# Kernel tuning notes

Hardware: AMD Instinct MI355X
Metric: run time of the kernel (lower is better)

The kernel has to match this reference:

```python
import jax, jax.numpy as jnp
import numpy as np

BETA = 0.25
N_CODEBOOK = 2  # hard-coded in the original module
EPS = 1e-12     # torch F.normalize default eps


def l2norm(t):
    # matches torch.nn.functional.normalize(t, p=2, dim=-1)
    n = jnp.linalg.norm(t, axis=-1, keepdims=True)
    return t / jnp.maximum(n, EPS)


def setup_inputs() -> dict:
    key = jax.random.key(0)
    k1, k2 = jax.random.split(key)
    b, n, e_dim, n_e = 16, 256, 1024, 4096
    c = e_dim // N_CODEBOOK
    z = jax.random.normal(k1, (b, n, e_dim), dtype=jnp.float32)
    emb_weight = jax.random.normal(k2, (N_CODEBOOK * n_e, c), dtype=jnp.float32)
    return {"z": z, "emb_weight": emb_weight}


def reference(z, emb_weight):
    b, n, e_dim = z.shape
    f = N_CODEBOOK
    c = e_dim // f
    n_e = emb_weight.shape[0] // f

    # 'b n (f c) -> b f n c'
    zf = jnp.transpose(z.reshape(b, n, f, c), (0, 2, 1, 3))
    # '(b f) c -> b f c' with b=2 (codebooks), f=n_e
    protos = emb_weight.reshape(f, n_e, c)

    zn = l2norm(zf)            # (b, f, n, c)
    pn = l2norm(protos)        # (f, m, c)

    # cosine distance; batch repeat of prototypes is a pure broadcast
    d = 2.0 - 2.0 * jnp.einsum('bfnc,fmc->bfnm', zn, pn)  # (b, f, n, m)
    encoding_indices = jnp.argmin(d, axis=-1)              # (b, f, n) in [0, n_e)

    # faithful to source: indices gather from the FULL (2*n_e) table, no offset
    z_q = l2norm(emb_weight[encoding_indices])             # (b, f, n, c)

    sg = jax.lax.stop_gradient
    loss = BETA * jnp.mean((sg(z_q) - zn) ** 2) + jnp.mean((z_q - sg(zn)) ** 2)

    z_q_st = zn + sg(z_q - zn)                             # straight-through
    # 'b f n c -> b n (f c)'
    z_q_out = jnp.transpose(z_q_st, (0, 2, 1, 3)).reshape(b, n, e_dim)
    return z_q_out, loss, encoding_indices
```

## Files before the change

### kernel.cpp

```cpp
#include <hip/hip_runtime.h>
#include <hip/hip_bf16.h>
#include <stdint.h>

#define FCB 2
#define BB 16
#define NN 256
#define EDIM 1024
#define CC 512
#define NE 4096
#define TOKENS (BB*FCB*NN)
#define ROWS (FCB*NE)
#define OUT_LOSS (BB*NN*EDIM)
#define OUT_IDX  (OUT_LOSS + 1)
#define MARGIN 0.15f

typedef __attribute__((ext_vector_type(8))) short bf16x8;
typedef __attribute__((ext_vector_type(4))) float f32x4;

__device__ __forceinline__ unsigned int ford(float v) {
    unsigned int u = __float_as_uint(v);
    return (u & 0x80000000u) ? ~u : (u | 0x80000000u);
}
__device__ __forceinline__ float unford(unsigned int u) {
    unsigned int b = (u & 0x80000000u) ? (u & 0x7fffffffu) : ~u;
    return __uint_as_float(b);
}


__global__ __launch_bounds__(256) void pack_hi(
    const float* __restrict__ z, const float* __restrict__ emb,
    short* __restrict__ z_hi, short* __restrict__ e_hi,
    float* __restrict__ norm_sq)
{
    __shared__ float red[256];
    int bid = blockIdx.x;
    int tid = threadIdx.x;
    bool is_emb = (bid >= 2048);
    const float* src; short* hi; int RS, FRO, FCO;
    if (!is_emb) { src = z;   hi = z_hi; RS = EDIM; FRO = 0;  FCO = CC; }
    else         { src = emb; hi = e_hi; RS = CC;   FRO = NE; FCO = 0; bid -= 2048; }
    int u = bid * 256 + tid;
    int m = u & 15;
    int Q = (u >> 4) & 63;
    int R = (u >> 10) & 255;
    int f = u >> 18;
    int row = R * 16 + m;
    const float* s = src + (size_t)(f * FRO + row) * RS + f * FCO + Q * 8;
    float4 v0 = *(const float4*)s;
    float4 v1 = *(const float4*)(s + 4);
    float vv[8] = {v0.x, v0.y, v0.z, v0.w, v1.x, v1.y, v1.z, v1.w};
    bf16x8 h8;
    float ss = 0.f;
    #pragma unroll
    for (int j = 0; j < 8; ++j) {
        __hip_bfloat16 hb = __float2bfloat16(vv[j]);
        h8[j] = *(short*)&hb;
        ss = fmaf(vv[j], vv[j], ss);
    }
    *(bf16x8*)(hi + (size_t)u * 8) = h8;

    if (is_emb) {
        red[tid] = ss;
        __syncthreads();
        if (tid < 16) {
            float t = 0.f;
            #pragma unroll
            for (int q = 0; q < 16; ++q) t += red[tid + 16 * q];
            int bf = (bid * 256) >> 18;
            int bR = ((bid * 256) >> 10) & 255;
            atomicAdd(norm_sq + bf * NE + bR * 16 + tid, t);
        }
    }
}

__global__ __launch_bounds__(256, 3) void gemm_sel(
    const short* __restrict__ zh, const short* __restrict__ eh,
    const float* __restrict__ norm_sq, unsigned int* __restrict__ cand)
{
    __shared__ char smem[32768];
    const int f  = blockIdx.z;
    const int t0 = blockIdx.y * 128;
    const int m0 = blockIdx.x * 128;
    const int tid  = threadIdx.x;
    const int wave = tid >> 6, lane = tid & 63;
    const int wm = wave & 1, wn = wave >> 1;

    f32x4 acc[4][4] = {};

    for (int step = 0; step < 8; ++step) {
        __syncthreads();
        #pragma unroll
        for (int i = 0; i < 8; ++i) {
            int c = wave * 8 + i;
            const short* gsrc = (c < 16) ? zh : eh;
            int cl = c & 15;
            int Rl = cl >> 1, h = cl & 1;
            int R = ((c < 16) ? (t0 >> 4) : (m0 >> 4)) + Rl;
            int qb = step * 8 + h * 4;
            const short* g = gsrc
                + (((size_t)f * 256 + R) * 64 + qb) * 128 + (size_t)lane * 8;
            __builtin_amdgcn_global_load_lds(
                (const __attribute__((address_space(1))) void*)g,
                (__attribute__((address_space(3))) void*)(smem + c * 1024),
                16, 0, 0);
        }
        __syncthreads();

        #pragma unroll
        for (int h = 0; h < 2; ++h) {
            bf16x8 ah[4], bh[4];
            #pragma unroll
            for (int i = 0; i < 4; ++i) {
                ah[i] = *(const bf16x8*)(smem + ((wm*4 + i)*2 + h) * 1024 + lane * 16);
                bh[i] = *(const bf16x8*)(smem + 16384 + ((wn*4 + i)*2 + h) * 1024 + lane * 16);
            }
            #pragma unroll
            for (int i = 0; i < 4; ++i)
                #pragma unroll
                for (int j2 = 0; j2 < 4; ++j2)
                    acc[i][j2] = __builtin_amdgcn_mfma_f32_16x16x32_bf16(ah[i], bh[j2], acc[i][j2], 0, 0, 0);
        }
    }

    float inm[4]; unsigned ccode[4];
    #pragma unroll
    for (int j2 = 0; j2 < 4; ++j2) {
        int col = j2 * 16 + (lane & 15);
        ccode[j2] = (unsigned)(col ^ 63);
        inm[j2] = rsqrtf(norm_sq[f * NE + m0 + wn * 64 + col]);
    }

    #pragma unroll
    for (int i = 0; i < 4; ++i) {
        #pragma unroll
        for (int r = 0; r < 4; ++r) {
            unsigned p1 = 0u, p2 = 0u;
            #pragma unroll
            for (int j2 = 0; j2 < 4; ++j2) {
                float w = acc[i][j2][r] * inm[j2];
                unsigned pw = (ford(w) & 0xFFFFFFC0u) | ccode[j2];
                if (pw > p1) { p2 = p1; p1 = pw; }
                else if (pw > p2) p2 = pw;
            }
            #pragma unroll
            for (int off = 8; off; off >>= 1) {
                unsigned q1 = __shfl_down(p1, off, 16);
                unsigned q2 = __shfl_down(p2, off, 16);
                if (q1 > p1) { unsigned t = p1; p1 = q1; p2 = (t > q2) ? t : q2; }
                else         { p2 = (p2 > q1) ? p2 : q1; }
            }
            if ((lane & 15) == 0) {
                int u = t0 + wm * 64 + i * 16 + (lane >> 4) * 4 + r;
                int b = u >> 8, n = u & 255;
                int gt = ((b * FCB + f) << 8) + n;
                int s = (blockIdx.x << 1) | wn;
                uint2 val; val.x = p1; val.y = p2;
                *(uint2*)(cand + ((size_t)gt << 7) + (s << 1)) = val;
            }
        }
    }
}

__global__ __launch_bounds__(256) void rescore_epilogue(
    const float* __restrict__ z, const float* __restrict__ emb,
    const unsigned int* __restrict__ cand,
    float* __restrict__ out, float* __restrict__ loss_tok)
{
    int t = blockIdx.x * 4 + (threadIdx.x >> 6);
    int lane = threadIdx.x & 63;
    int n = t & 255;
    int f = (t >> 8) & 1;
    int b = t >> 9;
    const float* zrow = z + ((size_t)(b*NN + n))*EDIM + f*CC;
    float4 za = *(const float4*)(zrow + lane * 8);
    float4 zb = *(const float4*)(zrow + lane * 8 + 4);

    uint2 cc = *(const uint2*)(cand + ((size_t)t << 7) + (lane << 1));
    unsigned c1 = cc.x, c2 = cc.y;

    unsigned m1 = (c1 > c2) ? c1 : c2;
    #pragma unroll
    for (int off = 32; off; off >>= 1) {
        unsigned o = __shfl_xor(m1, off);
        if (o > m1) m1 = o;
    }
    float thr = unford(m1) - MARGIN;

    unsigned long long bestp = 0ull;
    #pragma unroll
    for (int rnd = 0; rnd < 2; ++rnd) {
        unsigned u = rnd ? c2 : c1;
        float v = unford(u);
        unsigned long long mask = __ballot(v > thr);
        while (mask) {
            int src = __ffsll((long long)mask) - 1;
            mask &= mask - 1;
            unsigned cu = __shfl(u, src);
            int idx = (src << 6) | ((int)(cu & 63u) ^ 63);
            const float* er = emb + ((size_t)(f * NE + idx)) * CC;
            float4 ea = *(const float4*)(er + lane * 8);
            float4 eb = *(const float4*)(er + lane * 8 + 4);
            float d  = za.x*ea.x + za.y*ea.y + za.z*ea.z + za.w*ea.w
                     + zb.x*eb.x + zb.y*eb.y + zb.z*eb.z + zb.w*eb.w;
            float se = ea.x*ea.x + ea.y*ea.y + ea.z*ea.z + ea.w*ea.w
                     + eb.x*eb.x + eb.y*eb.y + eb.z*eb.z + eb.w*eb.w;
            #pragma unroll
            for (int off = 32; off; off >>= 1) {
                d  += __shfl_xor(d, off);
                se += __shfl_xor(se, off);
            }
            float vex = d / fmaxf(sqrtf(se), 1e-12f);
            unsigned long long pex = ((unsigned long long)ford(vex) << 32)
                                   | (unsigned int)(~(unsigned int)idx);
            if (pex > bestp) bestp = pex;
        }
    }
    int idxb = (int)(~(unsigned int)bestp);

    const float* er0 = emb + (size_t)idxb * CC;
    float4 ea = *(const float4*)(er0 + lane * 8);
    float4 eb = *(const float4*)(er0 + lane * 8 + 4);
    float se0 = ea.x*ea.x + ea.y*ea.y + ea.z*ea.z + ea.w*ea.w
              + eb.x*eb.x + eb.y*eb.y + eb.z*eb.z + eb.w*eb.w;
    #pragma unroll
    for (int off = 32; off; off >>= 1) se0 += __shfl_xor(se0, off);
    float inm0 = 1.0f / fmaxf(sqrtf(se0), 1e-12f);
    float* orow = out + ((size_t)(b*NN + n))*EDIM + f*CC;
    ea.x *= inm0; ea.y *= inm0; ea.z *= inm0; ea.w *= inm0;
    eb.x *= inm0; eb.y *= inm0; eb.z *= inm0; eb.w *= inm0;
    *(float4*)(orow + lane * 8) = ea;
    *(float4*)(orow + lane * 8 + 4) = eb;
    float s1 = za.x*za.x + za.y*za.y + za.z*za.z + za.w*za.w
             + zb.x*zb.x + zb.y*zb.y + zb.z*zb.z + zb.w*zb.w;
    float s2 = za.x*ea.x + za.y*ea.y + za.z*ea.z + za.w*ea.w
             + zb.x*eb.x + zb.y*eb.y + zb.z*eb.z + zb.w*eb.w;
    #pragma unroll
    for (int off = 32; off; off >>= 1) {
        s1 += __shfl_xor(s1, off);
        s2 += __shfl_xor(s2, off);
    }
    if (lane == 0) {
        float cosv = s2 / fmaxf(sqrtf(s1), 1e-12f);
        loss_tok[t] = 2.0f - 2.0f * cosv;
        out[OUT_IDX + t] = (float)idxb;
    }
}

__global__ __launch_bounds__(256) void loss_reduce(
    const float* __restrict__ loss_tok, float* __restrict__ out)
{
    int tid = threadIdx.x;
    float s = 0.f;
    #pragma unroll
    for (int h = 0; h < 32; ++h) s += loss_tok[h * 256 + tid];
    #pragma unroll
    for (int off = 32; off; off >>= 1) s += __shfl_down(s, off);
    __shared__ float part[4];
    if ((tid & 63) == 0) part[tid >> 6] = s;
    __syncthreads();
    if (tid == 0) {
        float t = part[0] + part[1] + part[2] + part[3];
        out[OUT_LOSS] = t * (1.25f / (float)OUT_LOSS);
    }
}

extern "C" void kernel_launch(void* const* d_in, const int* in_sizes, int n_in,
                              void* d_out, int out_size, void* d_ws, size_t ws_size,
                              hipStream_t stream) {
    const float* z   = (const float*)d_in[0];
    const float* emb = (const float*)d_in[1];
    float* out = (float*)d_out;

    char* ws = (char*)d_ws;
    float* norm_sq = (float*)ws;
    unsigned int* cand = (unsigned int*)(ws + 32768);
    float* loss_tok = (float*)(ws + 32768 + (size_t)4*1024*1024);
    short* z_hi = (short*)(ws + 65536 + (size_t)4*1024*1024);
    short* e_hi = z_hi + (size_t)FCB * NE * CC;

    hipMemsetAsync(norm_sq, 0, ROWS * sizeof(float), stream);
    pack_hi<<<4096, 256, 0, stream>>>(z, emb, z_hi, e_hi, norm_sq);
    gemm_sel<<<dim3(NE/128, NE/128, FCB), 256, 0, stream>>>(z_hi, e_hi, norm_sq, cand);
    rescore_epilogue<<<TOKENS/4, 256, 0, stream>>>(z, emb, cand, out, loss_tok);
    loss_reduce<<<1, 256, 0, stream>>>(loss_tok, out);
}
```

Baseline: 146.3 us.

## Enlarge similarity GEMM tile to 256x256 with double-buffered async LDS pipeline

Rewrites the bf16 similarity GEMM to use 256x256 block tiles with 8 waves. The main loop is now software-pipelined: global_load_lds prefetches the next K-chunk into a second 64KB LDS buffer while MFMAs run on the current one. Fine-grained vmcnt waits, explicit barriers and s_setprio bracket the MFMA bursts. The aim is to raise operand reuse and hide global-load latency. In exchange it uses 128KB of LDS per block, which limits occupancy to one block per CU, and halves the grid size, so tail effects can grow.

```diff
diff --git a/kernel.cpp b/kernel.cpp
--- a/kernel.cpp
+++ b/kernel.cpp
@@ -25,6 +25,11 @@
     unsigned int b = (u & 0x80000000u) ? (u & 0x7fffffffu) : ~u;
     return __uint_as_float(b);
 }
+
+__device__ __forceinline__ void vm8()   { asm volatile("s_waitcnt vmcnt(8)" ::: "memory"); }
+__device__ __forceinline__ void vm4()   { asm volatile("s_waitcnt vmcnt(4)" ::: "memory"); }
+__device__ __forceinline__ void vm0()   { asm volatile("s_waitcnt vmcnt(0)" ::: "memory"); }
+__device__ __forceinline__ void lgkm0() { asm volatile("s_waitcnt lgkmcnt(0)" ::: "memory"); }
 
 
 __global__ __launch_bounds__(256) void pack_hi(
@@ -73,72 +78,137 @@
     }
 }
 
-__global__ __launch_bounds__(256, 3) void gemm_sel(
+__global__ __launch_bounds__(512, 2) void gemm_sel(
     const short* __restrict__ zh, const short* __restrict__ eh,
     const float* __restrict__ norm_sq, unsigned int* __restrict__ cand)
 {
-    __shared__ char smem[32768];
+    __shared__ __attribute__((aligned(128))) char smem[131072];
     const int f  = blockIdx.z;
-    const int t0 = blockIdx.y * 128;
-    const int m0 = blockIdx.x * 128;
+    const int t0 = blockIdx.y * 256;
+    const int m0 = blockIdx.x * 256;
     const int tid  = threadIdx.x;
     const int wave = tid >> 6, lane = tid & 63;
     const int wm = wave & 1, wn = wave >> 1;
 
-    f32x4 acc[4][4] = {};
-
-    for (int step = 0; step < 8; ++step) {
-        __syncthreads();
-        #pragma unroll
-        for (int i = 0; i < 8; ++i) {
-            int c = wave * 8 + i;
-            const short* gsrc = (c < 16) ? zh : eh;
-            int cl = c & 15;
-            int Rl = cl >> 1, h = cl & 1;
-            int R = ((c < 16) ? (t0 >> 4) : (m0 >> 4)) + Rl;
-            int qb = step * 8 + h * 4;
-            const short* g = gsrc
-                + (((size_t)f * 256 + R) * 64 + qb) * 128 + (size_t)lane * 8;
+    const int cbA = (f * 256 + (t0 >> 4)) * 64;
+    const int cbB = (f * 256 + (m0 >> 4)) * 64;
+
+    f32x4 acc[8][4] = {};
+
+    auto stage_half = [&](const short* __restrict__ gsrc, int chunk0, char* dst) {
+        #pragma unroll
+        for (int i = 0; i < 2; ++i) {
+            int Rp = wave * 2 + i;
+            const short* g = gsrc + ((size_t)(chunk0 + Rp * 64)) * 128 + (size_t)lane * 8;
             __builtin_amdgcn_global_load_lds(
                 (const __attribute__((address_space(1))) void*)g,
-                (__attribute__((address_space(3))) void*)(smem + c * 1024),
-                16, 0, 0);
+                (__attribute__((address_space(3))) void*)(dst + Rp * 1024), 16, 0, 0);
         }
-        __syncthreads();
-
-        #pragma unroll
-        for (int h = 0; h < 2; ++h) {
-            bf16x8 ah[4], bh[4];
-            #pragma unroll
-            for (int i = 0; i < 4; ++i) {
-                ah[i] = *(const bf16x8*)(smem + ((wm*4 + i)*2 + h) * 1024 + lane * 16);
-                bh[i] = *(const bf16x8*)(smem + 16384 + ((wn*4 + i)*2 + h) * 1024 + lane * 16);
-            }
-            #pragma unroll
-            for (int i = 0; i < 4; ++i)
-                #pragma unroll
-                for (int j2 = 0; j2 < 4; ++j2)
-                    acc[i][j2] = __builtin_amdgcn_mfma_f32_16x16x32_bf16(ah[i], bh[j2], acc[i][j2], 0, 0, 0);
-        }
+    };
+
+    stage_half(zh, cbA + 0,     smem + 0);
+    stage_half(eh, cbB + 0,     smem + 32768);
+    stage_half(zh, cbA + 4,     smem + 16384);
+    stage_half(eh, cbB + 4,     smem + 32768 + 16384);
+    stage_half(zh, cbA + 8,     smem + 65536);
+    stage_half(eh, cbB + 8,     smem + 65536 + 32768);
+    vm8();
+    __builtin_amdgcn_s_barrier();
+
+    #pragma unroll
+    for (int t = 0; t < 8; ++t) {
+        char* cur = smem + (t & 1) * 65536;
+        char* nxt = smem + ((t + 1) & 1) * 65536;
+        const char* curA = cur;
+        const char* curB = cur + 32768;
+        bf16x8 af[4], bf[4];
+
+        #pragma unroll
+        for (int nj = 0; nj < 4; ++nj)
+            bf[nj] = *(const bf16x8*)(curB + (wn * 4 + nj) * 1024 + lane * 16);
+        #pragma unroll
+        for (int mi = 0; mi < 4; ++mi)
+            af[mi] = *(const bf16x8*)(curA + (wm * 8 + mi) * 1024 + lane * 16);
+        if (t < 7) stage_half(zh, cbA + (t + 1) * 8 + 4, nxt + 16384);
+        __builtin_amdgcn_s_barrier();
+        lgkm0();
+        __builtin_amdgcn_s_setprio(1);
+        #pragma unroll
+        for (int mi = 0; mi < 4; ++mi)
+            #pragma unroll
+            for (int nj = 0; nj < 4; ++nj)
+                acc[mi][nj] = __builtin_amdgcn_mfma_f32_16x16x32_bf16(af[mi], bf[nj], acc[mi][nj], 0, 0, 0);
+        __builtin_amdgcn_s_setprio(0);
+        __builtin_amdgcn_s_barrier();
+
+        #pragma unroll
+        for (int mi = 0; mi < 4; ++mi)
+            af[mi] = *(const bf16x8*)(curA + (wm * 8 + 4 + mi) * 1024 + lane * 16);
+        if (t < 7) stage_half(eh, cbB + (t + 1) * 8 + 4, nxt + 32768 + 16384);
+        if (t < 7) vm8(); else vm0();
+        __builtin_amdgcn_s_barrier();
+        lgkm0();
+        __builtin_amdgcn_s_setprio(1);
+        #pragma unroll
+        for (int mi = 0; mi < 4; ++mi)
+            #pragma unroll
+            for (int nj = 0; nj < 4; ++nj)
+                acc[4 + mi][nj] = __builtin_amdgcn_mfma_f32_16x16x32_bf16(af[mi], bf[nj], acc[4 + mi][nj], 0, 0, 0);
+        __builtin_amdgcn_s_setprio(0);
+        __builtin_amdgcn_s_barrier();
+
+        #pragma unroll
+        for (int nj = 0; nj < 4; ++nj)
+            bf[nj] = *(const bf16x8*)(curB + 16384 + (wn * 4 + nj) * 1024 + lane * 16);
+        #pragma unroll
+        for (int mi = 0; mi < 4; ++mi)
+            af[mi] = *(const bf16x8*)(curA + 16384 + (wm * 8 + mi) * 1024 + lane * 16);
+        if (t < 6) stage_half(zh, cbA + (t + 2) * 8, cur);
+        __builtin_amdgcn_s_barrier();
+        lgkm0();
+        __builtin_amdgcn_s_setprio(1);
+        #pragma unroll
+        for (int mi = 0; mi < 4; ++mi)
+            #pragma unroll
+            for (int nj = 0; nj < 4; ++nj)
+                acc[mi][nj] = __builtin_amdgcn_mfma_f32_16x16x32_bf16(af[mi], bf[nj], acc[mi][nj], 0, 0, 0);
+        __builtin_amdgcn_s_setprio(0);
+        __builtin_amdgcn_s_barrier();
+
+        #pragma unroll
+        for (int mi = 0; mi < 4; ++mi)
+            af[mi] = *(const bf16x8*)(curA + 16384 + (wm * 8 + 4 + mi) * 1024 + lane * 16);
+        if (t < 6) stage_half(eh, cbB + (t + 2) * 8, cur + 32768);
+        if (t < 6) vm8(); else if (t == 6) vm4();
+        __builtin_amdgcn_s_barrier();
+        lgkm0();
+        __builtin_amdgcn_s_setprio(1);
+        #pragma unroll
+        for (int mi = 0; mi < 4; ++mi)
+            #pragma unroll
+            for (int nj = 0; nj < 4; ++nj)
+                acc[4 + mi][nj] = __builtin_amdgcn_mfma_f32_16x16x32_bf16(af[mi], bf[nj], acc[4 + mi][nj], 0, 0, 0);
+        __builtin_amdgcn_s_setprio(0);
+        __builtin_amdgcn_s_barrier();
     }
 
     float inm[4]; unsigned ccode[4];
     #pragma unroll
-    for (int j2 = 0; j2 < 4; ++j2) {
-        int col = j2 * 16 + (lane & 15);
-        ccode[j2] = (unsigned)(col ^ 63);
-        inm[j2] = rsqrtf(norm_sq[f * NE + m0 + wn * 64 + col]);
-    }
-
-    #pragma unroll
-    for (int i = 0; i < 4; ++i) {
+    for (int nj = 0; nj < 4; ++nj) {
+        int col = nj * 16 + (lane & 15);
+        ccode[nj] = (unsigned)(col ^ 63);
+        inm[nj] = rsqrtf(norm_sq[f * NE + m0 + wn * 64 + col]);
+    }
+
+    #pragma unroll
+    for (int mi = 0; mi < 8; ++mi) {
         #pragma unroll
         for (int r = 0; r < 4; ++r) {
             unsigned p1 = 0u, p2 = 0u;
             #pragma unroll
-            for (int j2 = 0; j2 < 4; ++j2) {
-                float w = acc[i][j2][r] * inm[j2];
-                unsigned pw = (ford(w) & 0xFFFFFFC0u) | ccode[j2];
+            for (int nj = 0; nj < 4; ++nj) {
+                float w = acc[mi][nj][r] * inm[nj];
+                unsigned pw = (ford(w) & 0xFFFFFFC0u) | ccode[nj];
                 if (pw > p1) { p2 = p1; p1 = pw; }
                 else if (pw > p2) p2 = pw;
             }
@@ -146,14 +216,14 @@
             for (int off = 8; off; off >>= 1) {
                 unsigned q1 = __shfl_down(p1, off, 16);
                 unsigned q2 = __shfl_down(p2, off, 16);
-                if (q1 > p1) { unsigned t = p1; p1 = q1; p2 = (t > q2) ? t : q2; }
+                if (q1 > p1) { unsigned tt = p1; p1 = q1; p2 = (tt > q2) ? tt : q2; }
                 else         { p2 = (p2 > q1) ? p2 : q1; }
             }
             if ((lane & 15) == 0) {
-                int u = t0 + wm * 64 + i * 16 + (lane >> 4) * 4 + r;
+                int u = t0 + wm * 128 + mi * 16 + (lane >> 4) * 4 + r;
                 int b = u >> 8, n = u & 255;
                 int gt = ((b * FCB + f) << 8) + n;
-                int s = (blockIdx.x << 1) | wn;
+                int s = (blockIdx.x << 2) | wn;
                 uint2 val; val.x = p1; val.y = p2;
                 *(uint2*)(cand + ((size_t)gt << 7) + (s << 1)) = val;
             }
@@ -280,7 +350,7 @@
 
     hipMemsetAsync(norm_sq, 0, ROWS * sizeof(float), stream);
     pack_hi<<<4096, 256, 0, stream>>>(z, emb, z_hi, e_hi, norm_sq);
-    gemm_sel<<<dim3(NE/128, NE/128, FCB), 256, 0, stream>>>(z_hi, e_hi, norm_sq, cand);
+    gemm_sel<<<dim3(NE/256, NE/256, FCB), 512, 0, stream>>>(z_hi, e_hi, norm_sq, cand);
     rescore_epilogue<<<TOKENS/4, 256, 0, stream>>>(z, emb, cand, out, loss_tok);
     loss_reduce<<<1, 256, 0, stream>>>(loss_tok, out);
 }
```

New measurement: 144.3 us. About the same (-1.3%).

## Double-buffer GEMM LDS staging with 256-token tiles and fuse loss reduction via atomics

Applied to the files above, without the earlier changes.

The selection GEMM now uses 512-thread blocks covering 256 tokens by 128 codebook rows. LDS staging is split into two half-buffers so the next K-step's global-to-LDS loads are issued before the current MFMAs run, which is meant to hide load latency and drop one barrier per step. The separate loss-reduce kernel is removed: each token atomically adds its scaled loss into the output after a memset, saving a launch. The cost is more LDS per block and heavier register pressure, plus a nondeterministic float atomic sum contended by all 8192 tokens.

```diff
diff --git a/kernel.cpp b/kernel.cpp
--- a/kernel.cpp
+++ b/kernel.cpp
@@ -73,72 +73,81 @@
     }
 }
 
-__global__ __launch_bounds__(256, 3) void gemm_sel(
+__global__ __launch_bounds__(512, 4) void gemm_sel(
     const short* __restrict__ zh, const short* __restrict__ eh,
     const float* __restrict__ norm_sq, unsigned int* __restrict__ cand)
 {
-    __shared__ char smem[32768];
+    __shared__ __attribute__((aligned(128))) char smem[49152];
     const int f  = blockIdx.z;
-    const int t0 = blockIdx.y * 128;
+    const int t0 = blockIdx.y * 256;
     const int m0 = blockIdx.x * 128;
     const int tid  = threadIdx.x;
     const int wave = tid >> 6, lane = tid & 63;
-    const int wm = wave & 1, wn = wave >> 1;
+    const int wm = wave & 3, wn = wave >> 2;
 
     f32x4 acc[4][4] = {};
 
-    for (int step = 0; step < 8; ++step) {
-        __syncthreads();
+    auto stage = [&](int t, int h) {
+        int qb = t * 8 + h * 4;
+        char* base = smem + h * 24576;
         #pragma unroll
-        for (int i = 0; i < 8; ++i) {
-            int c = wave * 8 + i;
-            const short* gsrc = (c < 16) ? zh : eh;
-            int cl = c & 15;
-            int Rl = cl >> 1, h = cl & 1;
-            int R = ((c < 16) ? (t0 >> 4) : (m0 >> 4)) + Rl;
-            int qb = step * 8 + h * 4;
-            const short* g = gsrc
-                + (((size_t)f * 256 + R) * 64 + qb) * 128 + (size_t)lane * 8;
+        for (int i = 0; i < 2; ++i) {
+            int Rl = wave * 2 + i;
+            const short* g = zh + (((size_t)f * 256 + (t0 >> 4) + Rl) * 64 + qb) * 128
+                           + (size_t)lane * 8;
             __builtin_amdgcn_global_load_lds(
                 (const __attribute__((address_space(1))) void*)g,
-                (__attribute__((address_space(3))) void*)(smem + c * 1024),
-                16, 0, 0);
-        }
-        __syncthreads();
-
+                (__attribute__((address_space(3))) void*)(base + Rl * 1024), 16, 0, 0);
+        }
+        const short* g = eh + (((size_t)f * 256 + (m0 >> 4) + wave) * 64 + qb) * 128
+                       + (size_t)lane * 8;
+        __builtin_amdgcn_global_load_lds(
+            (const __attribute__((address_space(1))) void*)g,
+            (__attribute__((address_space(3))) void*)(base + 16384 + wave * 1024), 16, 0, 0);
+    };
+
+    stage(0, 0);
+    stage(0, 1);
+    __syncthreads();
+
+    for (int t = 0; t < 8; ++t) {
         #pragma unroll
         for (int h = 0; h < 2; ++h) {
-            bf16x8 ah[4], bh[4];
-            #pragma unroll
-            for (int i = 0; i < 4; ++i) {
-                ah[i] = *(const bf16x8*)(smem + ((wm*4 + i)*2 + h) * 1024 + lane * 16);
-                bh[i] = *(const bf16x8*)(smem + 16384 + ((wn*4 + i)*2 + h) * 1024 + lane * 16);
-            }
-            #pragma unroll
-            for (int i = 0; i < 4; ++i)
+            const char* base = smem + h * 24576;
+            bf16x8 af[4], bfr[4];
+            #pragma unroll
+            for (int mi = 0; mi < 4; ++mi)
+                af[mi] = *(const bf16x8*)(base + (wm * 4 + mi) * 1024 + lane * 16);
+            #pragma unroll
+            for (int nj = 0; nj < 4; ++nj)
+                bfr[nj] = *(const bf16x8*)(base + 16384 + (wn * 4 + nj) * 1024 + lane * 16);
+            __syncthreads();
+            if (t < 7) stage(t + 1, h);
+            #pragma unroll
+            for (int mi = 0; mi < 4; ++mi)
                 #pragma unroll
-                for (int j2 = 0; j2 < 4; ++j2)
-                    acc[i][j2] = __builtin_amdgcn_mfma_f32_16x16x32_bf16(ah[i], bh[j2], acc[i][j2], 0, 0, 0);
+                for (int nj = 0; nj < 4; ++nj)
+                    acc[mi][nj] = __builtin_amdgcn_mfma_f32_16x16x32_bf16(af[mi], bfr[nj], acc[mi][nj], 0, 0, 0);
         }
     }
 
     float inm[4]; unsigned ccode[4];
     #pragma unroll
-    for (int j2 = 0; j2 < 4; ++j2) {
-        int col = j2 * 16 + (lane & 15);
-        ccode[j2] = (unsigned)(col ^ 63);
-        inm[j2] = rsqrtf(norm_sq[f * NE + m0 + wn * 64 + col]);
-    }
-
-    #pragma unroll
-    for (int i = 0; i < 4; ++i) {
+    for (int nj = 0; nj < 4; ++nj) {
+        int col = nj * 16 + (lane & 15);
+        ccode[nj] = (unsigned)(col ^ 63);
+        inm[nj] = rsqrtf(norm_sq[f * NE + m0 + wn * 64 + col]);
+    }
+
+    #pragma unroll
+    for (int mi = 0; mi < 4; ++mi) {
         #pragma unroll
         for (int r = 0; r < 4; ++r) {
             unsigned p1 = 0u, p2 = 0u;
             #pragma unroll
-            for (int j2 = 0; j2 < 4; ++j2) {
-                float w = acc[i][j2][r] * inm[j2];
-                unsigned pw = (ford(w) & 0xFFFFFFC0u) | ccode[j2];
+            for (int nj = 0; nj < 4; ++nj) {
+                float w = acc[mi][nj][r] * inm[nj];
+                unsigned pw = (ford(w) & 0xFFFFFFC0u) | ccode[nj];
                 if (pw > p1) { p2 = p1; p1 = pw; }
                 else if (pw > p2) p2 = pw;
             }
@@ -146,11 +155,11 @@
             for (int off = 8; off; off >>= 1) {
                 unsigned q1 = __shfl_down(p1, off, 16);
                 unsigned q2 = __shfl_down(p2, off, 16);
-                if (q1 > p1) { unsigned t = p1; p1 = q1; p2 = (t > q2) ? t : q2; }
+                if (q1 > p1) { unsigned tt = p1; p1 = q1; p2 = (tt > q2) ? tt : q2; }
                 else         { p2 = (p2 > q1) ? p2 : q1; }
             }
             if ((lane & 15) == 0) {
-                int u = t0 + wm * 64 + i * 16 + (lane >> 4) * 4 + r;
+                int u = t0 + wm * 64 + mi * 16 + (lane >> 4) * 4 + r;
                 int b = u >> 8, n = u & 255;
                 int gt = ((b * FCB + f) << 8) + n;
                 int s = (blockIdx.x << 1) | wn;
@@ -163,8 +172,7 @@
 
 __global__ __launch_bounds__(256) void rescore_epilogue(
     const float* __restrict__ z, const float* __restrict__ emb,
-    const unsigned int* __restrict__ cand,
-    float* __restrict__ out, float* __restrict__ loss_tok)
+    const unsigned int* __restrict__ cand, float* __restrict__ out)
 {
     int t = blockIdx.x * 4 + (threadIdx.x >> 6);
     int lane = threadIdx.x & 63;
@@ -241,26 +249,9 @@
     }
     if (lane == 0) {
         float cosv = s2 / fmaxf(sqrtf(s1), 1e-12f);
-        loss_tok[t] = 2.0f - 2.0f * cosv;
+        float loss = 2.0f - 2.0f * cosv;
+        atomicAdd(out + OUT_LOSS, loss * (1.25f / (float)OUT_LOSS));
         out[OUT_IDX + t] = (float)idxb;
-    }
-}
-
-__global__ __launch_bounds__(256) void loss_reduce(
-    const float* __restrict__ loss_tok, float* __restrict__ out)
-{
-    int tid = threadIdx.x;
-    float s = 0.f;
-    #pragma unroll
-    for (int h = 0; h < 32; ++h) s += loss_tok[h * 256 + tid];
-    #pragma unroll
-    for (int off = 32; off; off >>= 1) s += __shfl_down(s, off);
-    __shared__ float part[4];
-    if ((tid & 63) == 0) part[tid >> 6] = s;
-    __syncthreads();
-    if (tid == 0) {
-        float t = part[0] + part[1] + part[2] + part[3];
-        out[OUT_LOSS] = t * (1.25f / (float)OUT_LOSS);
     }
 }
 
@@ -274,13 +265,12 @@
     char* ws = (char*)d_ws;
     float* norm_sq = (float*)ws;
     unsigned int* cand = (unsigned int*)(ws + 32768);
-    float* loss_tok = (float*)(ws + 32768 + (size_t)4*1024*1024);
     short* z_hi = (short*)(ws + 65536 + (size_t)4*1024*1024);
     short* e_hi = z_hi + (size_t)FCB * NE * CC;
 
     hipMemsetAsync(norm_sq, 0, ROWS * sizeof(float), stream);
+    hipMemsetAsync(out + OUT_LOSS, 0, sizeof(float), stream);
     pack_hi<<<4096, 256, 0, stream>>>(z, emb, z_hi, e_hi, norm_sq);
-    gemm_sel<<<dim3(NE/128, NE/128, FCB), 256, 0, stream>>>(z_hi, e_hi, norm_sq, cand);
-    rescore_epilogue<<<TOKENS/4, 256, 0, stream>>>(z, emb, cand, out, loss_tok);
-    loss_reduce<<<1, 256, 0, stream>>>(loss_tok, out);
-}
+    gemm_sel<<<dim3(NE/128, 4096/256, FCB), 512, 0, stream>>>(z_hi, e_hi, norm_sq, cand);
+    rescore_epilogue<<<TOKENS/4, 256, 0, stream>>>(z, emb, cand, out);
+}
```

New measurement: 242.3 us. +65.6%, slower.

## Double-buffer GEMM LDS staging and reuse precomputed norms in rescore

Applied to the files above, without the earlier changes.

Splits the GEMM's shared-memory tile into two buffers so the next K-step's global-to-LDS loads are issued before computing on the current buffer. Launch bounds are relaxed from 3 to 2 blocks per CU to fit the doubled LDS. The rescore kernel now reads squared codebook norms already accumulated by the pack kernel, instead of recomputing and reducing them for each candidate and for the final row. The tradeoff is lower occupancy in the GEMM, and the norms come from an atomic accumulation rather than a direct reduction.

```diff
diff --git a/kernel.cpp b/kernel.cpp
--- a/kernel.cpp
+++ b/kernel.cpp
@@ -73,11 +73,11 @@
     }
 }
 
-__global__ __launch_bounds__(256, 3) void gemm_sel(
+__global__ __launch_bounds__(256, 2) void gemm_sel(
     const short* __restrict__ zh, const short* __restrict__ eh,
     const float* __restrict__ norm_sq, unsigned int* __restrict__ cand)
 {
-    __shared__ char smem[32768];
+    __shared__ __attribute__((aligned(128))) char smem[2][32768];
     const int f  = blockIdx.z;
     const int t0 = blockIdx.y * 128;
     const int m0 = blockIdx.x * 128;
@@ -87,8 +87,7 @@
 
     f32x4 acc[4][4] = {};
 
-    for (int step = 0; step < 8; ++step) {
-        __syncthreads();
+    auto stage = [&](int step, char* dst) {
         #pragma unroll
         for (int i = 0; i < 8; ++i) {
             int c = wave * 8 + i;
@@ -101,18 +100,26 @@
                 + (((size_t)f * 256 + R) * 64 + qb) * 128 + (size_t)lane * 8;
             __builtin_amdgcn_global_load_lds(
                 (const __attribute__((address_space(1))) void*)g,
-                (__attribute__((address_space(3))) void*)(smem + c * 1024),
+                (__attribute__((address_space(3))) void*)(dst + c * 1024),
                 16, 0, 0);
         }
-        __syncthreads();
+    };
+
+    stage(0, smem[0]);
+    __syncthreads();
+
+    #pragma unroll
+    for (int step = 0; step < 8; ++step) {
+        const char* cur = smem[step & 1];
+        if (step < 7) stage(step + 1, smem[(step & 1) ^ 1]);
 
         #pragma unroll
         for (int h = 0; h < 2; ++h) {
             bf16x8 ah[4], bh[4];
             #pragma unroll
             for (int i = 0; i < 4; ++i) {
-                ah[i] = *(const bf16x8*)(smem + ((wm*4 + i)*2 + h) * 1024 + lane * 16);
-                bh[i] = *(const bf16x8*)(smem + 16384 + ((wn*4 + i)*2 + h) * 1024 + lane * 16);
+                ah[i] = *(const bf16x8*)(cur + ((wm*4 + i)*2 + h) * 1024 + lane * 16);
+                bh[i] = *(const bf16x8*)(cur + 16384 + ((wn*4 + i)*2 + h) * 1024 + lane * 16);
             }
             #pragma unroll
             for (int i = 0; i < 4; ++i)
@@ -120,6 +127,7 @@
                 for (int j2 = 0; j2 < 4; ++j2)
                     acc[i][j2] = __builtin_amdgcn_mfma_f32_16x16x32_bf16(ah[i], bh[j2], acc[i][j2], 0, 0, 0);
         }
+        __syncthreads();
     }
 
     float inm[4]; unsigned ccode[4];
@@ -163,7 +171,7 @@
 
 __global__ __launch_bounds__(256) void rescore_epilogue(
     const float* __restrict__ z, const float* __restrict__ emb,
-    const unsigned int* __restrict__ cand,
+    const unsigned int* __restrict__ cand, const float* __restrict__ norm_sq,
     float* __restrict__ out, float* __restrict__ loss_tok)
 {
     int t = blockIdx.x * 4 + (threadIdx.x >> 6);
@@ -202,13 +210,9 @@
             float4 eb = *(const float4*)(er + lane * 8 + 4);
             float d  = za.x*ea.x + za.y*ea.y + za.z*ea.z + za.w*ea.w
                      + zb.x*eb.x + zb.y*eb.y + zb.z*eb.z + zb.w*eb.w;
-            float se = ea.x*ea.x + ea.y*ea.y + ea.z*ea.z + ea.w*ea.w
-                     + eb.x*eb.x + eb.y*eb.y + eb.z*eb.z + eb.w*eb.w;
-            #pragma unroll
-            for (int off = 32; off; off >>= 1) {
-                d  += __shfl_xor(d, off);
-                se += __shfl_xor(se, off);
-            }
+            #pragma unroll
+            for (int off = 32; off; off >>= 1) d += __shfl_xor(d, off);
+            float se = norm_sq[f * NE + idx];
             float vex = d / fmaxf(sqrtf(se), 1e-12f);
             unsigned long long pex = ((unsigned long long)ford(vex) << 32)
                                    | (unsigned int)(~(unsigned int)idx);
@@ -220,11 +224,7 @@
     const float* er0 = emb + (size_t)idxb * CC;
     float4 ea = *(const float4*)(er0 + lane * 8);
     float4 eb = *(const float4*)(er0 + lane * 8 + 4);
-    float se0 = ea.x*ea.x + ea.y*ea.y + ea.z*ea.z + ea.w*ea.w
-              + eb.x*eb.x + eb.y*eb.y + eb.z*eb.z + eb.w*eb.w;
-    #pragma unroll
-    for (int off = 32; off; off >>= 1) se0 += __shfl_xor(se0, off);
-    float inm0 = 1.0f / fmaxf(sqrtf(se0), 1e-12f);
+    float inm0 = 1.0f / fmaxf(sqrtf(norm_sq[idxb]), 1e-12f);
     float* orow = out + ((size_t)(b*NN + n))*EDIM + f*CC;
     ea.x *= inm0; ea.y *= inm0; ea.z *= inm0; ea.w *= inm0;
     eb.x *= inm0; eb.y *= inm0; eb.z *= inm0; eb.w *= inm0;
@@ -281,6 +281,6 @@
     hipMemsetAsync(norm_sq, 0, ROWS * sizeof(float), stream);
     pack_hi<<<4096, 256, 0, stream>>>(z, emb, z_hi, e_hi, norm_sq);
     gemm_sel<<<dim3(NE/128, NE/128, FCB), 256, 0, stream>>>(z_hi, e_hi, norm_sq, cand);
-    rescore_epilogue<<<TOKENS/4, 256, 0, stream>>>(z, emb, cand, out, loss_tok);
+    rescore_epilogue<<<TOKENS/4, 256, 0, stream>>>(z, emb, cand, norm_sq, out, loss_tok);
     loss_reduce<<<1, 256, 0, stream>>>(loss_tok, out);
 }
```

New measurement: 149.5 us. +2.2%, slower.
